# Kernel optimization log

Hardware: AMD Instinct MI355X
Metric: run time of the kernel (lower is better)

## Reference

```python
import jax, jax.numpy as jnp
import numpy as np

N = 8_000_000   # total nodes (atoms)
B = 4096        # number of graphs in the batch
EPS = 1e-05


def setup_inputs() -> dict:
    key = jax.random.key(0)
    k1, k2 = jax.random.split(key)
    pos = jax.random.normal(k1, (N, 3), dtype=jnp.float32)
    batch = jnp.sort(jax.random.randint(k2, (N,), 0, B).astype(jnp.int64))
    weight = jnp.ones((1, 1), dtype=jnp.float32)
    return {"pos": pos, "batch": batch, "weight": weight}


def reference(pos, batch, weight):
    # per-node L2 norm of 3D coordinates -> [N, 1]
    norm = jnp.linalg.norm(pos, axis=-1, keepdims=True)
    # scatter_mean over graphs: segment sums of norms and counts -> [B, 1]
    seg_sum = jax.ops.segment_sum(norm, batch, num_segments=B)
    counts = jax.ops.segment_sum(jnp.ones_like(norm), batch, num_segments=B)
    mean_norm = seg_sum / jnp.maximum(counts, 1.0)  # empty segments -> 0 (matches scatter_mean)
    # gather per-graph mean back to nodes and normalize
    new_pos = weight * pos / (mean_norm[batch] + EPS)
    return new_pos
```

## Files before the change

### kernel.cpp

```cpp
#include <hip/hip_runtime.h>

#define EPS_F 1e-5f
#define BGRAPHS 4096
#define NPB 1024
#define WIN 8
#define ENC 0x40000000
#define INF_I 0x7fffffff

__device__ __forceinline__ int batch_shift(const int* __restrict__ batch, int n) {
    return (batch[n - 1] == 0) ? 1 : 0;
}

__global__ __launch_bounds__(256) void se3_seg_reduce(
    const float* __restrict__ pos, const int* __restrict__ batch,
    float* __restrict__ sums, float* __restrict__ cnts,
    int* __restrict__ enc, int n)
{
    const int tid  = blockIdx.x * blockDim.x + threadIdx.x;
    const int base = tid * 4;
    const int lane = threadIdx.x & 63;
    const int shift = batch_shift(batch, n);

    int   cur_b = -1;
    float cur_s = 0.f, cur_c = 0.f;

    if (base < n) {
        int   b4[4];
        float nrm[4];
        int   prev;
        const int nb = min(4, n - base);
        if (nb == 4) {
            if (shift == 0) {
                const int4 bi = *reinterpret_cast<const int4*>(batch + base);
                b4[0] = bi.x; b4[1] = bi.y; b4[2] = bi.z; b4[3] = bi.w;
            } else {
                const int4 v0 = *reinterpret_cast<const int4*>(batch + 2 * base);
                const int4 v1 = *reinterpret_cast<const int4*>(batch + 2 * base + 4);
                b4[0] = v0.x; b4[1] = v0.z; b4[2] = v1.x; b4[3] = v1.z;
            }
            const int up = __shfl_up(b4[3], 1);
            if (lane == 0) prev = (base == 0) ? -1 : batch[(size_t)(base - 1) << shift];
            else           prev = up;

            const float4* p = reinterpret_cast<const float4*>(pos + (size_t)base * 3);
            const float4 a = p[0], b = p[1], c = p[2];
            nrm[0] = sqrtf(a.x * a.x + a.y * a.y + a.z * a.z);
            nrm[1] = sqrtf(a.w * a.w + b.x * b.x + b.y * b.y);
            nrm[2] = sqrtf(b.z * b.z + b.w * b.w + c.x * c.x);
            nrm[3] = sqrtf(c.y * c.y + c.z * c.z + c.w * c.w);
        } else {
            for (int j = 0; j < 4; ++j) { b4[j] = -1; nrm[j] = 0.f; }
            for (int j = 0; j < nb; ++j) {
                b4[j] = batch[(size_t)(base + j) << shift];
                const float x = pos[(size_t)(base + j) * 3 + 0];
                const float y = pos[(size_t)(base + j) * 3 + 1];
                const float z = pos[(size_t)(base + j) * 3 + 2];
                nrm[j] = sqrtf(x * x + y * y + z * z);
            }
            prev = (base == 0) ? -1 : batch[(size_t)(base - 1) << shift];
        }

        if (b4[0] >= 0 && b4[0] != prev) enc[b4[0]] = ENC - base;
        #pragma unroll
        for (int j = 1; j < 4; ++j)
            if (b4[j] >= 0 && b4[j] != b4[j - 1]) enc[b4[j]] = ENC - (base + j);

        cur_b = b4[0];
        cur_s = nrm[0];
        cur_c = (b4[0] >= 0) ? 1.f : 0.f;
        #pragma unroll
        for (int j = 1; j < 4; ++j) {
            if (b4[j] == cur_b) { cur_s += nrm[j]; cur_c += 1.f; }
            else {
                if (cur_b >= 0) { atomicAdd(&sums[cur_b], cur_s); atomicAdd(&cnts[cur_b], cur_c); }
                cur_b = b4[j]; cur_s = nrm[j]; cur_c = (b4[j] >= 0) ? 1.f : 0.f;
            }
        }
    }

    #pragma unroll
    for (int off = 1; off < 64; off <<= 1) {
        const float os = __shfl_down(cur_s, off);
        const float oc = __shfl_down(cur_c, off);
        const int   ob = __shfl_down(cur_b, off);
        if (lane + off < 64 && ob == cur_b) { cur_s += os; cur_c += oc; }
    }
    const int pb = __shfl_up(cur_b, 1);
    if ((lane == 0 || pb != cur_b) && cur_b >= 0) {
        atomicAdd(&sums[cur_b], cur_s);
        atomicAdd(&cnts[cur_b], cur_c);
    }
}

__global__ __launch_bounds__(1024) void se3_finalize(
    const float* __restrict__ sums, const float* __restrict__ cnts,
    const float* __restrict__ w, float* __restrict__ scale,
    int* __restrict__ enc, int* __restrict__ cg, int nchunks)
{
    __shared__ int ta[BGRAPHS], tb[BGRAPHS];
    const int t = threadIdx.x;
    for (int i = t; i < BGRAPHS; i += 1024) ta[i] = enc[i];
    __syncthreads();
    int* src = ta; int* dst = tb;
    for (int stride = 1; stride < BGRAPHS; stride <<= 1) {
        for (int i = t; i < BGRAPHS; i += 1024) {
            int v = src[i];
            if (i + stride < BGRAPHS) v = max(v, src[i + stride]);
            dst[i] = v;
        }
        __syncthreads();
        int* tmp = src; src = dst; dst = tmp;
    }
    for (int i = t; i < BGRAPHS; i += 1024) {
        enc[i] = ENC - src[i];
        const float mean = sums[i] / fmaxf(cnts[i], 1.f);
        scale[i] = w[0] / (mean + EPS_F);
    }
    for (int c = t; c < nchunks; c += 1024) {
        const int key = ENC - c * NPB;
        int lo = 0, hi = BGRAPHS - 1;
        #pragma unroll
        for (int s = 0; s < 12; ++s) {
            const int mid = (lo + hi + 1) >> 1;
            if (src[mid] >= key) lo = mid; else hi = mid - 1;
        }
        cg[c] = lo;
    }
}

__global__ __launch_bounds__(256) void se3_apply(
    const float* __restrict__ pos, const int* __restrict__ tstart,
    const float* __restrict__ scale, const int* __restrict__ cg,
    float* __restrict__ out, int n)
{
    const int base = (blockIdx.x * blockDim.x + threadIdx.x) * 4;
    if (base >= n) return;

    const int g0 = cg[blockIdx.x];
    int   w[WIN];
    float sw[WIN + 1];
    #pragma unroll
    for (int k = 0; k < WIN; ++k) {
        const int idx = g0 + 1 + k;
        w[k] = (idx < BGRAPHS) ? tstart[idx] : INF_I;
    }
    #pragma unroll
    for (int k = 0; k <= WIN; ++k) sw[k] = scale[min(g0 + k, BGRAPHS - 1)];

    float sc[4];
    #pragma unroll
    for (int j = 0; j < 4; ++j) {
        const int i = base + j;
        float s = sw[0];
        #pragma unroll
        for (int k = 0; k < WIN; ++k) s = (w[k] <= i) ? sw[k + 1] : s;
        sc[j] = s;
    }

    if (base + 4 <= n) {
        const float4* p = reinterpret_cast<const float4*>(pos + (size_t)base * 3);
        const float4 a = p[0], b = p[1], c = p[2];
        float4* q = reinterpret_cast<float4*>(out + (size_t)base * 3);
        q[0] = make_float4(a.x * sc[0], a.y * sc[0], a.z * sc[0], a.w * sc[1]);
        q[1] = make_float4(b.x * sc[1], b.y * sc[1], b.z * sc[2], b.w * sc[2]);
        q[2] = make_float4(c.x * sc[2], c.y * sc[3], c.z * sc[3], c.w * sc[3]);
    } else {
        for (int j = 0; j < n - base; ++j) {
            out[(size_t)(base + j) * 3 + 0] = pos[(size_t)(base + j) * 3 + 0] * sc[j];
            out[(size_t)(base + j) * 3 + 1] = pos[(size_t)(base + j) * 3 + 1] * sc[j];
            out[(size_t)(base + j) * 3 + 2] = pos[(size_t)(base + j) * 3 + 2] * sc[j];
        }
    }
}

extern "C" void kernel_launch(void* const* d_in, const int* in_sizes, int n_in,
                              void* d_out, int out_size, void* d_ws, size_t ws_size,
                              hipStream_t stream)
{
    const float* pos   = (const float*)d_in[0];
    const int*   batch = (const int*)d_in[1];
    const float* w     = (const float*)d_in[2];
    float*       out   = (float*)d_out;
    const int    n     = in_sizes[1];

    float* sums  = (float*)d_ws;
    float* cnts  = sums + BGRAPHS;
    int*   enc   = (int*)(cnts + BGRAPHS);
    float* scale = (float*)(enc + BGRAPHS);
    int*   cg    = (int*)(scale + BGRAPHS);

    const int nthreads = (n + 3) / 4;
    const int blocks   = (nthreads + 255) / 256;

    hipMemsetAsync(d_ws, 0, 3 * BGRAPHS * sizeof(float), stream);

    se3_seg_reduce<<<blocks, 256, 0, stream>>>(pos, batch, sums, cnts, enc, n);
    se3_finalize<<<1, 1024, 0, stream>>>(sums, cnts, w, scale, enc, cg, blocks);
    se3_apply<<<blocks, 256, 0, stream>>>(pos, enc, scale, cg, out, n);
}
```

Measured before the change: 76.79 us.

## Replace single-block suffix-max finalize with multi-block direct-start binary search

Segment start indices are now written directly instead of encoded, and the single-block finalize kernel with its shared-memory suffix-max scan is replaced by a multi-block kernel that computes scales and binary-searches the starts array from global memory. The apply kernel shrinks its lookup window from 8 to 4 and makes the chunk's first graph index wave-uniform. This removes a serial one-block bottleneck and a smaller memset. The risk is correctness: empty graphs leave stale or zero start entries without the suffix-max fill, so the binary search can go wrong, and the narrower window only holds if few graph boundaries fall in each chunk.

After: 69.96 us. 8.9% less time.

```diff
diff --git a/kernel.cpp b/kernel.cpp
--- a/kernel.cpp
+++ b/kernel.cpp
@@ -3,8 +3,7 @@
 #define EPS_F 1e-5f
 #define BGRAPHS 4096
 #define NPB 1024
-#define WIN 8
-#define ENC 0x40000000
+#define WIN 4
 #define INF_I 0x7fffffff
 
 __device__ __forceinline__ int batch_shift(const int* __restrict__ batch, int n) {
@@ -14,7 +13,7 @@
 __global__ __launch_bounds__(256) void se3_seg_reduce(
     const float* __restrict__ pos, const int* __restrict__ batch,
     float* __restrict__ sums, float* __restrict__ cnts,
-    int* __restrict__ enc, int n)
+    int* __restrict__ starts, int n)
 {
     const int tid  = blockIdx.x * blockDim.x + threadIdx.x;
     const int base = tid * 4;
@@ -60,10 +59,10 @@
             prev = (base == 0) ? -1 : batch[(size_t)(base - 1) << shift];
         }
 
-        if (b4[0] >= 0 && b4[0] != prev) enc[b4[0]] = ENC - base;
+        if (b4[0] >= 0 && b4[0] != prev) starts[b4[0]] = base;
         #pragma unroll
         for (int j = 1; j < 4; ++j)
-            if (b4[j] >= 0 && b4[j] != b4[j - 1]) enc[b4[j]] = ENC - (base + j);
+            if (b4[j] >= 0 && b4[j] != b4[j - 1]) starts[b4[j]] = base + j;
 
         cur_b = b4[0];
         cur_s = nrm[0];
@@ -92,57 +91,43 @@
     }
 }
 
-__global__ __launch_bounds__(1024) void se3_finalize(
+__global__ __launch_bounds__(256) void se3_mid(
     const float* __restrict__ sums, const float* __restrict__ cnts,
-    const float* __restrict__ w, float* __restrict__ scale,
-    int* __restrict__ enc, int* __restrict__ cg, int nchunks)
+    const float* __restrict__ w, const int* __restrict__ starts,
+    float* __restrict__ scale, int* __restrict__ cg, int nchunks)
 {
-    __shared__ int ta[BGRAPHS], tb[BGRAPHS];
-    const int t = threadIdx.x;
-    for (int i = t; i < BGRAPHS; i += 1024) ta[i] = enc[i];
-    __syncthreads();
-    int* src = ta; int* dst = tb;
-    for (int stride = 1; stride < BGRAPHS; stride <<= 1) {
-        for (int i = t; i < BGRAPHS; i += 1024) {
-            int v = src[i];
-            if (i + stride < BGRAPHS) v = max(v, src[i + stride]);
-            dst[i] = v;
-        }
-        __syncthreads();
-        int* tmp = src; src = dst; dst = tmp;
-    }
-    for (int i = t; i < BGRAPHS; i += 1024) {
-        enc[i] = ENC - src[i];
+    const int i = blockIdx.x * blockDim.x + threadIdx.x;
+    if (i < BGRAPHS) {
         const float mean = sums[i] / fmaxf(cnts[i], 1.f);
         scale[i] = w[0] / (mean + EPS_F);
     }
-    for (int c = t; c < nchunks; c += 1024) {
-        const int key = ENC - c * NPB;
+    if (i < nchunks) {
+        const int x = i * NPB;
         int lo = 0, hi = BGRAPHS - 1;
         #pragma unroll
         for (int s = 0; s < 12; ++s) {
             const int mid = (lo + hi + 1) >> 1;
-            if (src[mid] >= key) lo = mid; else hi = mid - 1;
+            if (starts[mid] <= x) lo = mid; else hi = mid - 1;
         }
-        cg[c] = lo;
+        cg[i] = lo;
     }
 }
 
 __global__ __launch_bounds__(256) void se3_apply(
-    const float* __restrict__ pos, const int* __restrict__ tstart,
+    const float* __restrict__ pos, const int* __restrict__ starts,
     const float* __restrict__ scale, const int* __restrict__ cg,
     float* __restrict__ out, int n)
 {
     const int base = (blockIdx.x * blockDim.x + threadIdx.x) * 4;
     if (base >= n) return;
 
-    const int g0 = cg[blockIdx.x];
+    const int g0 = __builtin_amdgcn_readfirstlane(cg[blockIdx.x]);
     int   w[WIN];
     float sw[WIN + 1];
     #pragma unroll
     for (int k = 0; k < WIN; ++k) {
         const int idx = g0 + 1 + k;
-        w[k] = (idx < BGRAPHS) ? tstart[idx] : INF_I;
+        w[k] = (idx < BGRAPHS) ? starts[idx] : INF_I;
     }
     #pragma unroll
     for (int k = 0; k <= WIN; ++k) sw[k] = scale[min(g0 + k, BGRAPHS - 1)];
@@ -183,18 +168,19 @@
     float*       out   = (float*)d_out;
     const int    n     = in_sizes[1];
 
-    float* sums  = (float*)d_ws;
-    float* cnts  = sums + BGRAPHS;
-    int*   enc   = (int*)(cnts + BGRAPHS);
-    float* scale = (float*)(enc + BGRAPHS);
-    int*   cg    = (int*)(scale + BGRAPHS);
+    float* sums   = (float*)d_ws;
+    float* cnts   = sums + BGRAPHS;
+    int*   starts = (int*)(cnts + BGRAPHS);
+    float* scale  = (float*)(starts + BGRAPHS);
+    int*   cg     = (int*)(scale + BGRAPHS);
 
     const int nthreads = (n + 3) / 4;
     const int blocks   = (nthreads + 255) / 256;
 
-    hipMemsetAsync(d_ws, 0, 3 * BGRAPHS * sizeof(float), stream);
+    hipMemsetAsync(d_ws, 0, 2 * BGRAPHS * sizeof(float), stream);
 
-    se3_seg_reduce<<<blocks, 256, 0, stream>>>(pos, batch, sums, cnts, enc, n);
-    se3_finalize<<<1, 1024, 0, stream>>>(sums, cnts, w, scale, enc, cg, blocks);
-    se3_apply<<<blocks, 256, 0, stream>>>(pos, enc, scale, cg, out, n);
+    se3_seg_reduce<<<blocks, 256, 0, stream>>>(pos, batch, sums, cnts, starts, n);
+    const int midgrid = (max(BGRAPHS, blocks) + 255) / 256;
+    se3_mid<<<midgrid, 256, 0, stream>>>(sums, cnts, w, starts, scale, cg, blocks);
+    se3_apply<<<blocks, 256, 0, stream>>>(pos, starts, scale, cg, out, n);
 }
```
